# Kernel tuning notes

Measured on AMD Instinct MI355X. Metric: run time of the kernel, lower is better.

## Reference

```python
import math
import jax, jax.numpy as jnp
import numpy as np

EMBED = 1024
HEADS = 16
HEAD_DIM = EMBED // HEADS
NUM_BUCKETS = 32
MAX_DISTANCE = 128  # max_length
B, S = 2, 2048


def _relative_position_bucket(relative_position):
    # Faithful port of T5Attention._relative_position_bucket (bidirectional)
    num_buckets = NUM_BUCKETS // 2
    relative_buckets = (relative_position > 0).astype(jnp.int32) * num_buckets
    rp = jnp.abs(relative_position)
    max_exact = num_buckets // 2
    is_small = rp < max_exact
    # guard log(0); the small branch is selected where rp < max_exact anyway
    rel_if_large = max_exact + (
        jnp.log(jnp.maximum(rp, 1).astype(jnp.float32) / max_exact)
        / math.log(MAX_DISTANCE / max_exact)
        * (num_buckets - max_exact)
    ).astype(jnp.int32)
    rel_if_large = jnp.minimum(rel_if_large, num_buckets - 1)
    return relative_buckets + jnp.where(is_small, rp, rel_if_large)


def compute_bias(rel_bias_emb, seq_len):
    ctx = jnp.arange(seq_len)[:, None]
    mem = jnp.arange(seq_len)[None, :]
    rp_bucket = _relative_position_bucket(mem - ctx)          # [S, S]
    values = rel_bias_emb[rp_bucket]                          # [S, S, H]
    return jnp.transpose(values, (2, 0, 1))[None]             # [1, H, S, S]


def setup_inputs() -> dict:
    key = jax.random.key(0)
    ks = jax.random.split(key, 7)
    x = jax.random.normal(ks[0], (B, S, EMBED), dtype=jnp.float32)
    Wq = jax.random.normal(ks[1], (EMBED, EMBED), dtype=jnp.float32) * 0.02
    Wk = jax.random.normal(ks[2], (EMBED, EMBED), dtype=jnp.float32) * 0.02
    Wv = jax.random.normal(ks[3], (EMBED, EMBED), dtype=jnp.float32) * 0.02
    Wo = jax.random.normal(ks[4], (EMBED, EMBED), dtype=jnp.float32) * 0.02
    rel_bias_emb = jax.random.normal(ks[5], (NUM_BUCKETS, HEADS), dtype=jnp.float32) * 0.02
    key_pad_mask = jax.random.bernoulli(ks[6], 0.1, (B, S))  # True = padded key
    return {"x": x, "Wq": Wq, "Wk": Wk, "Wv": Wv, "Wo": Wo,
            "rel_bias_emb": rel_bias_emb, "key_pad_mask": key_pad_mask}


def reference(x, Wq, Wk, Wv, Wo, rel_bias_emb, key_pad_mask):
    Bsz, seq_len, _ = x.shape
    # nn.Linear(bias=False): y = x @ W.T
    q = (x @ Wq.T).reshape(Bsz, seq_len, HEADS, HEAD_DIM)
    k = (x @ Wk.T).reshape(Bsz, seq_len, HEADS, HEAD_DIM)
    v = (x @ Wv.T).reshape(Bsz, seq_len, HEADS, HEAD_DIM)
    scores = jnp.einsum("bqhd,bkhd->bhqk", q, k) / math.sqrt(HEAD_DIM)
    scores = scores + compute_bias(rel_bias_emb, seq_len)     # first layer only
    scores = jnp.where(key_pad_mask[:, None, None, :], -jnp.inf, scores)
    attn = jax.nn.softmax(scores, axis=-1)                    # dropout = identity (eval)
    out = jnp.einsum("bhqk,bkhd->bqhd", attn, v).reshape(Bsz, seq_len, EMBED)
    return out @ Wo.T
```

## Files before the change

### kernel.cpp

```cpp
#include <hip/hip_runtime.h>
#include <math.h>

#define BSZ 2
#define SEQ 2048
#define EMB 1024
#define NH 16
#define HD 64
#define NPOS (2*SEQ-1)
#define LOG2E 1.44269504f

typedef unsigned short ushortT;
typedef __attribute__((ext_vector_type(8)))  short short8v;
typedef __attribute__((ext_vector_type(16))) float f32x16;
typedef __attribute__((ext_vector_type(4)))  int   int4v;

#if __has_builtin(__builtin_amdgcn_exp2f)
#define EXP2(x) __builtin_amdgcn_exp2f(x)
#else
#define EXP2(x) exp2f(x)
#endif

#define MFMA32(a,b,c) __builtin_amdgcn_mfma_f32_32x32x16_bf16((a),(b),(c),0,0,0)

static __device__ inline unsigned bf16r(float x) {
    unsigned u = __builtin_bit_cast(unsigned, x);
    return (u + 0x7FFFu + ((u >> 16) & 1u)) >> 16;
}
static __device__ inline unsigned pkbf(float a, float b) {
    return bf16r(a) | (bf16r(b) << 16);
}

__global__ __launch_bounds__(256) void detect_kernel(const unsigned int* __restrict__ mw,
                                                     int* __restrict__ flag) {
    __shared__ int bad;
    if (threadIdx.x == 0) bad = 0;
    __syncthreads();
    int lb = 0;
    for (int i = threadIdx.x; i < (BSZ*SEQ)/4; i += 256) {
        unsigned int w = mw[i];
        if (w > 1u && w != 0x3F800000u) lb = 1;
    }
    if (lb) atomicOr(&bad, 1);
    __syncthreads();
    if (threadIdx.x == 0) *flag = bad;
}

__global__ __launch_bounds__(256) void mask_expand(const void* __restrict__ mask,
                                                   const int* __restrict__ flag,
                                                   float* __restrict__ mb) {
    int i = blockIdx.x * 256 + threadIdx.x;
    if (i >= BSZ*SEQ) return;
    int padded;
    if (*flag) padded = (((const unsigned char*)mask)[i] != 0);
    else       padded = (((const unsigned int*)mask)[i]  != 0u);
    mb[i] = padded ? -1e9f : 0.0f;
}

__global__ __launch_bounds__(256) void bias_table_kernel(const float* __restrict__ emb,
                                                         float* __restrict__ tab) {
    int i = blockIdx.x * 256 + threadIdx.x;
    if (i >= NH * NPOS) return;
    int h   = i / NPOS;
    int pos = i - h * NPOS;
    int rel = pos - (SEQ - 1);
    int rb  = rel > 0 ? 16 : 0;
    int rp  = rel < 0 ? -rel : rel;
    int val;
    if (rp < 8) {
        val = rp;
    } else {
        float t = logf((float)rp * 0.125f);
        t = t / (float)2.772588722239781;
        t = t * 8.0f;
        int li = (int)t;
        val = 8 + li;
        if (val > 15) val = 15;
    }
    tab[i] = emb[(rb + val) * NH + h] * LOG2E;
}

__global__ __launch_bounds__(256) void tobf16(const float* __restrict__ in,
                                              ushortT* __restrict__ outp, int n8) {
    int i = blockIdx.x * 256 + threadIdx.x;
    if (i >= n8) return;
    float4 a = ((const float4*)in)[2*i];
    float4 b = ((const float4*)in)[2*i+1];
    ((uint4*)outp)[i] = make_uint4(pkbf(a.x,a.y), pkbf(a.z,a.w),
                                   pkbf(b.x,b.y), pkbf(b.z,b.w));
}

template<int MODE>
__global__ __launch_bounds__(256) void gemm_mfma(const ushortT* __restrict__ A,
                                                 const ushortT* __restrict__ W,
                                                 void* __restrict__ Cout, float scale) {
    __shared__ ushortT smem[18432];
    ushortT* As = smem;
    ushortT* Bs = smem + 9216;
    const int t = threadIdx.x, lane = t & 63;
    const int w = t >> 6, wr = w >> 1, wc = w & 1;
    const int lq = lane & 31, hi = lane >> 5;
    const int m0 = blockIdx.y * 128, n0 = blockIdx.x * 128;

    f32x16 acc[2][2];
#pragma unroll
    for (int mr = 0; mr < 2; ++mr)
#pragma unroll
        for (int nc = 0; nc < 2; ++nc)
#pragma unroll
            for (int r = 0; r < 16; ++r) acc[mr][nc][r] = 0.f;

    const int ra0 = wr * 64 + lq, ra1 = ra0 + 32;
    const int rb0 = wc * 64 + lq, rb1 = rb0 + 32;

    for (int kt = 0; kt < 16; ++kt) {
        const int k0 = kt * 64;
        __syncthreads();
#pragma unroll
        for (int it = 0; it < 4; ++it) {
            int c   = t + it * 256;
            int row = c >> 3;
            int kc  = (c & 7) * 8;
            *(uint4*)&As[row * 72 + kc] = *(const uint4*)(A + (size_t)(m0 + row) * 1024 + k0 + kc);
            *(uint4*)&Bs[row * 72 + kc] = *(const uint4*)(W + (size_t)(n0 + row) * 1024 + k0 + kc);
        }
        __syncthreads();
#pragma unroll
        for (int ks = 0; ks < 4; ++ks) {
            int ca = ks * 16 + hi * 8;
            short8v a0 = *(const short8v*)&As[ra0 * 72 + ca];
            short8v a1 = *(const short8v*)&As[ra1 * 72 + ca];
            short8v b0 = *(const short8v*)&Bs[rb0 * 72 + ca];
            short8v b1 = *(const short8v*)&Bs[rb1 * 72 + ca];
            acc[0][0] = MFMA32(a0, b0, acc[0][0]);
            acc[0][1] = MFMA32(a0, b1, acc[0][1]);
            acc[1][0] = MFMA32(a1, b0, acc[1][0]);
            acc[1][1] = MFMA32(a1, b1, acc[1][1]);
        }
    }

    if (MODE == 2) {
        __syncthreads();
        ushortT* cs = smem;
#pragma unroll
        for (int mr = 0; mr < 2; ++mr)
#pragma unroll
            for (int nc = 0; nc < 2; ++nc) {
                int col = wc * 64 + nc * 32 + lq;
#pragma unroll
                for (int r = 0; r < 16; ++r) {
                    int row = wr * 64 + mr * 32 + (r & 3) + 8 * (r >> 2) + 4 * hi;
                    cs[row * 136 + col] = (ushortT)bf16r(acc[mr][nc][r] * scale);
                }
            }
        __syncthreads();
#pragma unroll
        for (int it = 0; it < 8; ++it) {
            int c   = t + it * 256;
            int row = c >> 4, cc = c & 15;
            uint4 v = *(const uint4*)&cs[row * 136 + cc * 8];
            int m = m0 + row, col = n0 + cc * 8;
            int b = m >> 11, s = m & (SEQ - 1);
            int h = col >> 6, d0 = col & 63;
            *(uint4*)((ushortT*)Cout + (((size_t)(b * NH + h) * SEQ + s) * HD + d0)) = v;
        }
    } else {
        float* cs = (float*)smem;
#pragma unroll
        for (int half = 0; half < 2; ++half) {
            __syncthreads();
            if (wr == half) {
#pragma unroll
                for (int mr = 0; mr < 2; ++mr)
#pragma unroll
                    for (int nc = 0; nc < 2; ++nc) {
                        int col = wc * 64 + nc * 32 + lq;
#pragma unroll
                        for (int r = 0; r < 16; ++r) {
                            int rl = mr * 32 + (r & 3) + 8 * (r >> 2) + 4 * hi;
                            cs[rl * 128 + col] = acc[mr][nc][r];
                        }
                    }
            }
            __syncthreads();
#pragma unroll
            for (int it = 0; it < 8; ++it) {
                int c   = t + it * 256;
                int row = c >> 5, cc = c & 31;
                float4 v = *(const float4*)&cs[row * 128 + cc * 4];
                *(float4*)((float*)Cout + (size_t)(m0 + half * 64 + row) * 1024 + n0 + cc * 4) = v;
            }
        }
    }
}

__global__ __launch_bounds__(256) void transpose_v(const ushortT* __restrict__ vin,
                                                   ushortT* __restrict__ vout) {
    __shared__ unsigned tile[64][65];
    const int s0 = blockIdx.x * 64;
    const int bh = blockIdx.y;
    const int t  = threadIdx.x;
#pragma unroll
    for (int it = 0; it < 2; ++it) {
        int idx = t + it * 256;
        int r   = idx >> 3;
        int c0  = (idx & 7) * 8;
        uint4 v = *(const uint4*)(vin + ((size_t)bh * SEQ + s0 + r) * HD + c0);
        unsigned a[4] = {v.x, v.y, v.z, v.w};
#pragma unroll
        for (int j = 0; j < 4; ++j) {
            tile[r][c0 + 2*j]     = a[j] & 0xFFFFu;
            tile[r][c0 + 2*j + 1] = a[j] >> 16;
        }
    }
    __syncthreads();
#pragma unroll
    for (int it = 0; it < 2; ++it) {
        int idx = t + it * 256;
        int d   = idx >> 3;
        int c0  = (idx & 7) * 8;
        unsigned wv[4];
#pragma unroll
        for (int j = 0; j < 4; ++j) {
            unsigned lo = tile[c0 + 2*j][d]     & 0xFFFFu;
            unsigned hv = tile[c0 + 2*j + 1][d] & 0xFFFFu;
            wv[j] = lo | (hv << 16);
        }
        *(uint4*)(vout + ((size_t)bh * HD + d) * SEQ + s0 + c0) = make_uint4(wv[0], wv[1], wv[2], wv[3]);
    }
}

__global__ __launch_bounds__(128) void flash_mfma(
    const ushortT* __restrict__ qb16, const ushortT* __restrict__ kb16,
    const ushortT* __restrict__ vt16, const float* __restrict__ tab,
    const float* __restrict__ maskb, ushortT* __restrict__ opb) {
    const int qt = blockIdx.x, h = blockIdx.y, b = blockIdx.z;
    const int qb0 = qt * 64;
    __shared__ float biasS[2112];
    __shared__ float maskS[2048];
    const int t = threadIdx.x, lane = t & 63, w = t >> 6;
    const int lq = lane & 31, hi = lane >> 5;

    for (int i = t; i < 2048; i += 128) maskS[i] = maskb[b * SEQ + i];
    for (int i = t; i < 2112; i += 128) {
        int ti = h * NPOS + i + 1984 - qb0;
        if (ti > NH * NPOS - 1) ti = NH * NPOS - 1;
        biasS[i] = tab[ti];
    }
    __syncthreads();

    const size_t bh = (size_t)b * NH + h;
    const ushortT* qp = qb16 + bh * SEQ * HD;
    const ushortT* kp = kb16 + bh * SEQ * HD;
    const ushortT* vp = vt16 + bh * SEQ * HD;

    const int qrow = qb0 + w * 32 + lq;
    short8v qf[4];
#pragma unroll
    for (int ds = 0; ds < 4; ++ds)
        qf[ds] = *(const short8v*)(qp + (size_t)qrow * HD + ds * 16 + hi * 8);

    f32x16 o0{}, o1{};
    float m_run = -1e30f, l_run = 0.f;
    const int bbase = 63 - w * 32 - lq;

    for (int k0 = 0; k0 < SEQ; k0 += 32) {
        short8v kf0 = *(const short8v*)(kp + (size_t)(k0 + lq) * HD +  0 + hi * 8);
        short8v kf1 = *(const short8v*)(kp + (size_t)(k0 + lq) * HD + 16 + hi * 8);
        short8v kf2 = *(const short8v*)(kp + (size_t)(k0 + lq) * HD + 32 + hi * 8);
        short8v kf3 = *(const short8v*)(kp + (size_t)(k0 + lq) * HD + 48 + hi * 8);

        f32x16 st;
#pragma unroll
        for (int rq = 0; rq < 4; ++rq) {
            int kb = k0 + 8 * rq + 4 * hi;
#pragma unroll
            for (int rr = 0; rr < 4; ++rr)
                st[4*rq + rr] = biasS[kb + bbase + rr] + maskS[kb + rr];
        }
        st = MFMA32(kf0, qf[0], st);
        st = MFMA32(kf1, qf[1], st);
        st = MFMA32(kf2, qf[2], st);
        st = MFMA32(kf3, qf[3], st);

        float pmax = st[0];
#pragma unroll
        for (int r = 1; r < 16; ++r) pmax = fmaxf(pmax, st[r]);
        pmax = fmaxf(pmax, __shfl_xor(pmax, 32));
        float grow = pmax - m_run;
        if (!__all(grow <= 8.0f)) {
            float mnew = fmaxf(m_run, pmax);
            float sc = EXP2(m_run - mnew);
            l_run *= sc;
#pragma unroll
            for (int r = 0; r < 16; ++r) {
                float scr = __shfl(sc, (r & 3) + 8 * (r >> 2) + 4 * hi);
                o0[r] *= scr; o1[r] *= scr;
            }
            m_run = mnew;
        }
        float p[16];
        float lt = 0.f;
#pragma unroll
        for (int r = 0; r < 16; ++r) { p[r] = EXP2(st[r] - m_run); lt += p[r]; }
        l_run += lt + __shfl_xor(lt, 32);

        unsigned x0 = pkbf(p[0],  p[1]),  y0 = pkbf(p[4],  p[5]);
        unsigned x1 = pkbf(p[2],  p[3]),  y1 = pkbf(p[6],  p[7]);
        unsigned x2 = pkbf(p[8],  p[9]),  y2 = pkbf(p[12], p[13]);
        unsigned x3 = pkbf(p[10], p[11]), y3 = pkbf(p[14], p[15]);
        unsigned sx0 = (unsigned)__shfl_xor((int)x0, 32), sy0 = (unsigned)__shfl_xor((int)y0, 32);
        unsigned sx1 = (unsigned)__shfl_xor((int)x1, 32), sy1 = (unsigned)__shfl_xor((int)y1, 32);
        unsigned sx2 = (unsigned)__shfl_xor((int)x2, 32), sy2 = (unsigned)__shfl_xor((int)y2, 32);
        unsigned sx3 = (unsigned)__shfl_xor((int)x3, 32), sy3 = (unsigned)__shfl_xor((int)y3, 32);
        bool lo = (lane < 32);
        int4v i0 = { (int)(lo ? x0 : sy0), (int)(lo ? x1 : sy1),
                     (int)(lo ? sx0 : y0), (int)(lo ? sx1 : y1) };
        int4v i1 = { (int)(lo ? x2 : sy2), (int)(lo ? x3 : sy3),
                     (int)(lo ? sx2 : y2), (int)(lo ? sx3 : y3) };
        short8v pa0 = __builtin_bit_cast(short8v, i0);
        short8v pa1 = __builtin_bit_cast(short8v, i1);

        short8v vf00 = *(const short8v*)(vp + (size_t)(lq)      * SEQ + k0 +  0 + hi * 8);
        short8v vf10 = *(const short8v*)(vp + (size_t)(lq)      * SEQ + k0 + 16 + hi * 8);
        short8v vf01 = *(const short8v*)(vp + (size_t)(32 + lq) * SEQ + k0 +  0 + hi * 8);
        short8v vf11 = *(const short8v*)(vp + (size_t)(32 + lq) * SEQ + k0 + 16 + hi * 8);
        o0 = MFMA32(pa0, vf00, o0);
        o0 = MFMA32(pa1, vf10, o0);
        o1 = MFMA32(pa0, vf01, o1);
        o1 = MFMA32(pa1, vf11, o1);
    }

#pragma unroll
    for (int r = 0; r < 16; ++r) {
        int rowq = (r & 3) + 8 * (r >> 2) + 4 * hi;
        float lr  = __shfl(l_run, rowq);
        float inv = 1.0f / lr;
        ushortT* dst = opb + ((size_t)b * SEQ + qb0 + w * 32 + rowq) * EMB + h * HD + lq;
        dst[0]  = (ushortT)bf16r(o0[r] * inv);
        dst[32] = (ushortT)bf16r(o1[r] * inv);
    }
}

extern "C" void kernel_launch(void* const* d_in, const int* in_sizes, int n_in,
                              void* d_out, int out_size, void* d_ws, size_t ws_size,
                              hipStream_t stream) {
    const float* x   = (const float*)d_in[0];
    const float* Wq  = (const float*)d_in[1];
    const float* Wk  = (const float*)d_in[2];
    const float* Wv  = (const float*)d_in[3];
    const float* Wo  = (const float*)d_in[4];
    const float* emb = (const float*)d_in[5];
    const void*  msk = d_in[6];
    char* wsb  = (char*)d_ws;
    float* out = (float*)d_out;

    const size_t MB = 1 << 20;
    int*     flag  = (int*)(wsb);
    float*   maskb = (float*)(wsb + 256);
    float*   tab   = (float*)(wsb + 16640);
    ushortT* xb    = (ushortT*)(wsb + 1*MB);
    ushortT* wqb   = (ushortT*)(wsb + 9*MB);
    ushortT* wkb   = (ushortT*)(wsb + 11*MB);
    ushortT* wvb   = (ushortT*)(wsb + 13*MB);
    ushortT* wob   = (ushortT*)(wsb + 15*MB);
    ushortT* qb16  = (ushortT*)(wsb + 17*MB);
    ushortT* kb16  = (ushortT*)(wsb + 25*MB);
    ushortT* vb16  = (ushortT*)(wsb + 33*MB);
    ushortT* vt16  = (ushortT*)(wsb + 41*MB);
    ushortT* opb   = (ushortT*)(wsb + 49*MB);

    detect_kernel<<<1, 256, 0, stream>>>((const unsigned int*)msk, flag);
    mask_expand<<<(BSZ*SEQ + 255) / 256, 256, 0, stream>>>(msk, flag, maskb);
    bias_table_kernel<<<(NH*NPOS + 255) / 256, 256, 0, stream>>>(emb, tab);

    const int n8x = BSZ*SEQ*EMB/8, n8w = EMB*EMB/8;
    tobf16<<<(n8x + 255)/256, 256, 0, stream>>>(x,  xb,  n8x);
    tobf16<<<(n8w + 255)/256, 256, 0, stream>>>(Wq, wqb, n8w);
    tobf16<<<(n8w + 255)/256, 256, 0, stream>>>(Wk, wkb, n8w);
    tobf16<<<(n8w + 255)/256, 256, 0, stream>>>(Wv, wvb, n8w);
    tobf16<<<(n8w + 255)/256, 256, 0, stream>>>(Wo, wob, n8w);

    dim3 g(EMB / 128, (BSZ * SEQ) / 128);
    const float qscale = 0.125f * LOG2E;
    gemm_mfma<2><<<g, 256, 0, stream>>>(xb, wqb, qb16, qscale);
    gemm_mfma<2><<<g, 256, 0, stream>>>(xb, wkb, kb16, 1.0f);
    gemm_mfma<2><<<g, 256, 0, stream>>>(xb, wvb, vb16, 1.0f);

    transpose_v<<<dim3(SEQ/64, BSZ*NH), 256, 0, stream>>>(vb16, vt16);

    flash_mfma<<<dim3(SEQ/64, NH, BSZ), 128, 0, stream>>>(qb16, kb16, vt16, tab, maskb, opb);

    gemm_mfma<0><<<g, 256, 0, stream>>>(opb, wob, out, 1.0f);
}
```

Measured before the change: 308.0 us.

## Split flash attention over key halves and combine partial softmax results

The attention kernel is split-K: each block processes half of the keys and writes unnormalized bf16 partial outputs plus running max and sum. A new combine kernel rescales and merges the two halves before the output projection. The aim is to double the number of attention blocks (from 1024 to 2048) for better occupancy on the many-CU GPU. The cost is extra global traffic for the partial outputs, one more launch, and an extra bf16 rounding of the unnormalized partials. Workspace buffers xb, vb16 and wqb are reused for these intermediates.

```diff
diff --git a/kernel.cpp b/kernel.cpp
--- a/kernel.cpp
+++ b/kernel.cpp
@@ -8,6 +8,7 @@
 #define HD 64
 #define NPOS (2*SEQ-1)
 #define LOG2E 1.44269504f
+#define KHALF 1024
 
 typedef unsigned short ushortT;
 typedef __attribute__((ext_vector_type(8)))  short short8v;
@@ -28,6 +29,9 @@
 }
 static __device__ inline unsigned pkbf(float a, float b) {
     return bf16r(a) | (bf16r(b) << 16);
+}
+static __device__ inline float bfu(unsigned hw) {
+    return __builtin_bit_cast(float, hw << 16);
 }
 
 __global__ __launch_bounds__(256) void detect_kernel(const unsigned int* __restrict__ mw,
@@ -232,8 +236,11 @@
 __global__ __launch_bounds__(128) void flash_mfma(
     const ushortT* __restrict__ qb16, const ushortT* __restrict__ kb16,
     const ushortT* __restrict__ vt16, const float* __restrict__ tab,
-    const float* __restrict__ maskb, ushortT* __restrict__ opb) {
-    const int qt = blockIdx.x, h = blockIdx.y, b = blockIdx.z;
+    const float* __restrict__ maskb,
+    ushortT* __restrict__ po0, ushortT* __restrict__ po1,
+    float2* __restrict__ ml) {
+    const int qt = blockIdx.x, h = blockIdx.y;
+    const int b = blockIdx.z >> 1, half = blockIdx.z & 1;
     const int qb0 = qt * 64;
     __shared__ float biasS[2112];
     __shared__ float maskS[2048];
@@ -263,7 +270,8 @@
     float m_run = -1e30f, l_run = 0.f;
     const int bbase = 63 - w * 32 - lq;
 
-    for (int k0 = 0; k0 < SEQ; k0 += 32) {
+    const int kbeg = half * KHALF, kend = kbeg + KHALF;
+    for (int k0 = kbeg; k0 < kend; k0 += 32) {
         short8v kf0 = *(const short8v*)(kp + (size_t)(k0 + lq) * HD +  0 + hi * 8);
         short8v kf1 = *(const short8v*)(kp + (size_t)(k0 + lq) * HD + 16 + hi * 8);
         short8v kf2 = *(const short8v*)(kp + (size_t)(k0 + lq) * HD + 32 + hi * 8);
@@ -330,15 +338,43 @@
         o1 = MFMA32(pa1, vf11, o1);
     }
 
+    ushortT* po = half ? po1 : po0;
 #pragma unroll
     for (int r = 0; r < 16; ++r) {
         int rowq = (r & 3) + 8 * (r >> 2) + 4 * hi;
-        float lr  = __shfl(l_run, rowq);
-        float inv = 1.0f / lr;
-        ushortT* dst = opb + ((size_t)b * SEQ + qb0 + w * 32 + rowq) * EMB + h * HD + lq;
-        dst[0]  = (ushortT)bf16r(o0[r] * inv);
-        dst[32] = (ushortT)bf16r(o1[r] * inv);
-    }
+        ushortT* dst = po + ((size_t)b * SEQ + qb0 + w * 32 + rowq) * EMB + h * HD + lq;
+        dst[0]  = (ushortT)bf16r(o0[r]);
+        dst[32] = (ushortT)bf16r(o1[r]);
+    }
+    if (hi == 0)
+        ml[(size_t)half * (BSZ*SEQ*NH) + ((size_t)b * SEQ + qb0 + w * 32 + lq) * NH + h] =
+            make_float2(m_run, l_run);
+}
+
+__global__ __launch_bounds__(256) void combine_halves(
+    const ushortT* __restrict__ po0, const ushortT* __restrict__ po1,
+    const float2* __restrict__ ml, ushortT* __restrict__ opb) {
+    int idx = blockIdx.x * 256 + threadIdx.x;
+    int e   = idx * 8;
+    int row = e >> 10;
+    int h   = (e & 1023) >> 6;
+    float2 ml0 = ml[(size_t)row * NH + h];
+    float2 ml1 = ml[(size_t)(BSZ*SEQ*NH) + (size_t)row * NH + h];
+    float ms = fmaxf(ml0.x, ml1.x);
+    float s0 = EXP2(ml0.x - ms), s1 = EXP2(ml1.x - ms);
+    float f  = 1.0f / (ml0.y * s0 + ml1.y * s1);
+    float f0 = s0 * f, f1 = s1 * f;
+    uint4 a = *(const uint4*)(po0 + e);
+    uint4 c = *(const uint4*)(po1 + e);
+    unsigned aw[4] = {a.x, a.y, a.z, a.w}, cw[4] = {c.x, c.y, c.z, c.w};
+    unsigned ow[4];
+#pragma unroll
+    for (int j = 0; j < 4; ++j) {
+        float r0 = bfu(aw[j] & 0xFFFFu) * f0 + bfu(cw[j] & 0xFFFFu) * f1;
+        float r1 = bfu(aw[j] >> 16)     * f0 + bfu(cw[j] >> 16)     * f1;
+        ow[j] = pkbf(r0, r1);
+    }
+    *(uint4*)(opb + e) = make_uint4(ow[0], ow[1], ow[2], ow[3]);
 }
 
 extern "C" void kernel_launch(void* const* d_in, const int* in_sizes, int n_in,
@@ -368,6 +404,9 @@
     ushortT* vb16  = (ushortT*)(wsb + 33*MB);
     ushortT* vt16  = (ushortT*)(wsb + 41*MB);
     ushortT* opb   = (ushortT*)(wsb + 49*MB);
+    ushortT* po0   = xb;
+    ushortT* po1   = vb16;
+    float2*  ml    = (float2*)wqb;
 
     detect_kernel<<<1, 256, 0, stream>>>((const unsigned int*)msk, flag);
     mask_expand<<<(BSZ*SEQ + 255) / 256, 256, 0, stream>>>(msk, flag, maskb);
@@ -388,7 +427,9 @@
 
     transpose_v<<<dim3(SEQ/64, BSZ*NH), 256, 0, stream>>>(vb16, vt16);
 
-    flash_mfma<<<dim3(SEQ/64, NH, BSZ), 128, 0, stream>>>(qb16, kb16, vt16, tab, maskb, opb);
+    flash_mfma<<<dim3(SEQ/64, NH, BSZ*2), 128, 0, stream>>>(qb16, kb16, vt16, tab, maskb,
+                                                            po0, po1, ml);
+    combine_halves<<<(BSZ*SEQ*EMB/8 + 255)/256, 256, 0, stream>>>(po0, po1, ml, opb);
 
     gemm_mfma<0><<<g, 256, 0, stream>>>(opb, wob, out, 1.0f);
 }
```

After: 338.2 us. +9.8%, slower.
